# Kernel optimization log

Hardware: AMD Instinct MI355X
Metric: run time of the kernel (lower is better)

## Reference

```python
import jax, jax.numpy as jnp
import numpy as np

B, T, D = 32, 4096, 768
HEADS, DK, DV = 4, 64, 64
REL_W = 32
HIDDEN = 256


def setup_inputs() -> dict:
    key = jax.random.key(0)
    ks = jax.random.split(key, 12)
    H_sent = jax.random.normal(ks[0], (B, T, D), dtype=jnp.float32)
    # realistic padding: each sample has a random valid length in [2048, T]
    lengths = jax.random.randint(ks[1], (B,), 2048, T + 1)
    attention_mask_sent = (jnp.arange(T)[None, :] < lengths[:, None]).astype(jnp.int32)
    noun_pos = jax.random.randint(ks[2], (B,), 0, 2048).astype(jnp.int32)
    pooled_fields = jax.random.normal(ks[3], (B, D), dtype=jnp.float32)
    # xavier-uniform for (heads, d, dk): fan_in=d, fan_out=dk per torch semantics
    def xavier(k, shape, fan_in, fan_out):
        lim = float(np.sqrt(6.0 / (fan_in + fan_out)))
        return jax.random.uniform(k, shape, jnp.float32, -lim, lim)
    WQ = xavier(ks[4], (HEADS, D, DK), D, DK)
    WK = xavier(ks[5], (HEADS, D, DK), D, DK)
    WV = xavier(ks[6], (HEADS, D, DV), D, DV)
    rel_bias = jnp.zeros((HEADS, 2 * REL_W + 1), jnp.float32) + 0.01 * jax.random.normal(ks[7], (HEADS, 2 * REL_W + 1))
    in_proj = D + HEADS * DV + D  # 1792
    proj_w = xavier(ks[8], (HIDDEN, in_proj), in_proj, HIDDEN)
    proj_b = jnp.zeros((HIDDEN,), jnp.float32)
    mlp_w = xavier(ks[9], (2, HIDDEN), HIDDEN, 2)
    mlp_b = jnp.zeros((2,), jnp.float32)
    return {
        "H_sent": H_sent, "attention_mask_sent": attention_mask_sent,
        "noun_pos": noun_pos, "pooled_fields": pooled_fields,
        "WQ": WQ, "WK": WK, "WV": WV, "rel_bias": rel_bias,
        "proj_w": proj_w, "proj_b": proj_b, "mlp_w": mlp_w, "mlp_b": mlp_b,
    }


def reference(H_sent, attention_mask_sent, noun_pos, pooled_fields,
              WQ, WK, WV, rel_bias, proj_w, proj_b, mlp_w, mlp_b):
    b, t, d = H_sent.shape
    heads, _, dk = WQ.shape
    w = (rel_bias.shape[1] - 1) // 2
    # gather single query vector per sample
    h_i = H_sent[jnp.arange(b), noun_pos]  # (B, d)
    Q = jnp.einsum('bd,hdk->bhk', h_i, WQ)        # (B, H, dk)
    K = jnp.einsum('btd,hdk->bthk', H_sent, WK)   # (B, T, H, dk)
    V = jnp.einsum('btd,hdv->bthv', H_sent, WV)   # (B, T, H, dv)
    scores = jnp.einsum('bhk,bthk->bht', Q, K) / jnp.sqrt(jnp.float32(dk))  # (B,H,T)
    # relative-position bias gathered by clamped delta
    delta = jnp.clip(jnp.arange(t)[None, :] - noun_pos[:, None], -w, w) + w  # (B,T)
    rb = rel_bias[:, delta]                        # (H, B, T)
    scores = scores + jnp.transpose(rb, (1, 0, 2))
    scores = jnp.where(attention_mask_sent[:, None, :] == 0, jnp.float32(-1e9), scores)
    alpha = jax.nn.softmax(scores, axis=-1)        # (B, H, T)
    c = jnp.einsum('bht,bthv->bhv', alpha, V).reshape(b, -1)  # (B, H*dv)
    r = jnp.concatenate([h_i, c, pooled_fields], axis=-1)     # (B, d + H*dv + d)
    hdn = jax.nn.gelu(r @ proj_w.T + proj_b, approximate=False)
    logits = hdn @ mlp_w.T + mlp_b                 # (B, 2)
    return logits
```

## Files before the change

### kernel.cpp

```cpp
#include <hip/hip_runtime.h>
#include <math.h>

#define BB 32
#define TT 4096
#define DD 768
#define NH 4
#define RELW 32
#define NREL 65
#define HIDDEN 256
#define INPROJ 1792

#define NCH 32
#define CROWS (TT / NCH)
#define TROWS 8
#define C4 (DD / 4)

#define WAITVM6() asm volatile("s_waitcnt vmcnt(6)" ::: "memory")
#define WAITVM0() asm volatile("s_waitcnt vmcnt(0)" ::: "memory")

__device__ __forceinline__ void gl_lds16(const float* g, float* l) {
    __builtin_amdgcn_global_load_lds(
        (const __attribute__((address_space(1))) float*)(uintptr_t)g,
        (__attribute__((address_space(3))) float*)(uintptr_t)l,
        16, 0, 0);
}

template <int CTRL, int RMASK>
__device__ __forceinline__ float upd0(float x) {
    return __int_as_float(__builtin_amdgcn_update_dpp(
        0, __float_as_int(x), CTRL, RMASK, 0xf, true));
}
__device__ __forceinline__ float wave_sum64(float x) {
    x += upd0<0x111, 0xf>(x);
    x += upd0<0x112, 0xf>(x);
    x += upd0<0x114, 0xf>(x);
    x += upd0<0x118, 0xf>(x);
    x += upd0<0x142, 0xa>(x);
    x += upd0<0x143, 0xc>(x);
    return __int_as_float(__builtin_amdgcn_readlane(__float_as_int(x), 63));
}

__global__ __launch_bounds__(256) void kA(const float* __restrict__ H,
                                          const int* __restrict__ noun_pos,
                                          const float* __restrict__ WQ,
                                          const float* __restrict__ WK,
                                          const float* __restrict__ pooled,
                                          float* __restrict__ R,
                                          float* __restrict__ qk_ws) {
    int b = blockIdx.x / NH, h = blockIdx.x % NH;
    __shared__ float hi_s[DD];
    __shared__ float qpart[4][64];
    __shared__ float q_s[64];
    int tn = noun_pos[b];
    const float* Hrow = H + ((size_t)b * TT + tn) * DD;
    for (int d = threadIdx.x; d < DD; d += 256) {
        float v = Hrow[d];
        hi_s[d] = v;
        if (h == 0) R[(size_t)b * INPROJ + d] = v;
        if (h == 1) R[(size_t)b * INPROJ + DD + NH * 64 + d] = pooled[(size_t)b * DD + d];
    }
    __syncthreads();
    {
        int k = threadIdx.x & 63, ds = threadIdx.x >> 6;
        const float* wq = WQ + (size_t)h * DD * 64 + k;
        float acc = 0.f;
        #pragma unroll 8
        for (int d = ds * 192; d < ds * 192 + 192; ++d) acc += hi_s[d] * wq[(size_t)d * 64];
        qpart[ds][k] = acc;
    }
    __syncthreads();
    if (threadIdx.x < 64)
        q_s[threadIdx.x] = qpart[0][threadIdx.x] + qpart[1][threadIdx.x]
                         + qpart[2][threadIdx.x] + qpart[3][threadIdx.x];
    __syncthreads();
    for (int d = threadIdx.x; d < DD; d += 256) {
        const float* wk = WK + ((size_t)h * DD + d) * 64;
        float acc = 0.f;
        #pragma unroll
        for (int k = 0; k < 64; ++k) acc += q_s[k] * wk[k];
        qk_ws[((size_t)b * NH + h) * DD + d] = acc * 0.125f;
    }
}

#define DOT(ACC, CV, QV) ACC += CV.x*QV.x + CV.y*QV.y + CV.z*QV.z + CV.w*QV.w

#define HUPD(M, L, S0, S1, B0, B1, B2)                                    \
  {                                                                        \
    float nm = fmaxf(M, fmaxf(S0, S1));                                    \
    if (nm > M + 8.0f) {                                                   \
      float sc = __expf(M - nm);                                           \
      L *= sc;                                                             \
      B0.x*=sc; B0.y*=sc; B0.z*=sc; B0.w*=sc;                              \
      B1.x*=sc; B1.y*=sc; B1.z*=sc; B1.w*=sc;                              \
      B2.x*=sc; B2.y*=sc; B2.z*=sc; B2.w*=sc;                              \
      M = nm;                                                              \
    }                                                                      \
    float p0 = __expf(S0 - M), p1 = __expf(S1 - M);                        \
    L += p0 + p1;                                                          \
    B0.x += p0*c0.x + p1*c3.x; B0.y += p0*c0.y + p1*c3.y;                  \
    B0.z += p0*c0.z + p1*c3.z; B0.w += p0*c0.w + p1*c3.w;                  \
    B1.x += p0*c1.x + p1*c4.x; B1.y += p0*c1.y + p1*c4.y;                  \
    B1.z += p0*c1.z + p1*c4.z; B1.w += p0*c1.w + p1*c4.w;                  \
    B2.x += p0*c2.x + p1*c5.x; B2.y += p0*c2.y + p1*c5.y;                  \
    B2.z += p0*c2.z + p1*c5.z; B2.w += p0*c2.w + p1*c5.w;                  \
  }

__global__ __launch_bounds__(256, 3) void kFlash(const float* __restrict__ H,
                                                 const int* __restrict__ mask,
                                                 const int* __restrict__ noun_pos,
                                                 const float* __restrict__ rel_bias,
                                                 const float* __restrict__ qk_ws,
                                                 float* __restrict__ macc,
                                                 float* __restrict__ ml) {
    const int b   = blockIdx.x / NCH;
    const int ch  = blockIdx.x % NCH;
    const int tid = threadIdx.x;
    const int wave = tid >> 6, lane = tid & 63;

    __shared__ float4 Hts[2][TROWS * C4];
    __shared__ float4 rbL[CROWS];
    __shared__ float mls[4][8];
    __shared__ int snl;

    const int t0 = ch * CROWS;
    const int tn = noun_pos[b];

    if (tid == 0) snl = 0;
    __syncthreads();
    if (tid < CROWS) {
        int t = t0 + tid;
        int dl = t - tn; dl = dl < -RELW ? -RELW : (dl > RELW ? RELW : dl);
        int mm = mask[(size_t)b * TT + t];
        float4 rv;
        if (mm) {
            rv.x = rel_bias[0 * NREL + dl + RELW];
            rv.y = rel_bias[1 * NREL + dl + RELW];
            rv.z = rel_bias[2 * NREL + dl + RELW];
            rv.w = rel_bias[3 * NREL + dl + RELW];
            atomicMax(&snl, tid + 1);
        } else {
            rv.x = rv.y = rv.z = rv.w = -2.0e9f;
        }
        rbL[tid] = rv;
    }

    float4 qr[NH][3];
    {
        const float4* qk4 = (const float4*)(qk_ws + (size_t)b * NH * DD);
        #pragma unroll
        for (int h = 0; h < NH; ++h)
            #pragma unroll
            for (int j = 0; j < 3; ++j)
                qr[h][j] = qk4[h * C4 + j * 64 + lane];
    }

    __syncthreads();
    const int NTE = (snl + TROWS - 1) / TROWS;

    if (NTE == 0) {
        float4 z = {0.f, 0.f, 0.f, 0.f};
        float4* mo = (float4*)(macc + (size_t)blockIdx.x * NH * DD);
        int h = tid >> 6, ln = tid & 63;
        #pragma unroll
        for (int j = 0; j < 3; ++j) mo[h * C4 + j * 64 + ln] = z;
        if (tid < NH) {
            float* mp = ml + (size_t)blockIdx.x * NH * 2;
            mp[tid * 2 + 0] = -3.0e38f; mp[tid * 2 + 1] = 0.f;
        }
        return;
    }

    float m0 = -3.0e38f, m1 = -3.0e38f, m2 = -3.0e38f, m3 = -3.0e38f;
    float l0 = 0.f, l1 = 0.f, l2 = 0.f, l3 = 0.f;
    float4 A00{0,0,0,0}, A01{0,0,0,0}, A02{0,0,0,0};
    float4 A10{0,0,0,0}, A11{0,0,0,0}, A12{0,0,0,0};
    float4 A20{0,0,0,0}, A21{0,0,0,0}, A22{0,0,0,0};
    float4 A30{0,0,0,0}, A31{0,0,0,0}, A32{0,0,0,0};

    const float* Hc = H + ((size_t)b * TT + t0) * DD;
    const int woff = wave * 1536;

    {
        float* dst = (float*)&Hts[0][0] + woff;
        const float* src = Hc + woff;
        #pragma unroll
        for (int i = 0; i < 6; ++i)
            gl_lds16(src + i * 256 + lane * 4, dst + i * 256);
    }

    #pragma unroll 1
    for (int t = 0; t < NTE; ++t) {
        const int cur = t & 1;
        if (t + 1 < NTE) {
            float* dst = (float*)&Hts[cur ^ 1][0] + woff;
            const float* src = Hc + (size_t)(t + 1) * TROWS * DD + woff;
            #pragma unroll
            for (int i = 0; i < 6; ++i)
                gl_lds16(src + i * 256 + lane * 4, dst + i * 256);
            WAITVM6();
        } else {
            WAITVM0();
        }
        const float4* Hr = &Hts[cur][0] + wave * 384;
        float4 c0 = Hr[lane],       c1 = Hr[64 + lane],  c2 = Hr[128 + lane];
        float4 c3 = Hr[192 + lane], c4 = Hr[256 + lane], c5 = Hr[320 + lane];

        float s00 = 0, s01 = 0, s02 = 0, s03 = 0;
        float s10 = 0, s11 = 0, s12 = 0, s13 = 0;
        DOT(s00, c0, qr[0][0]); DOT(s00, c1, qr[0][1]); DOT(s00, c2, qr[0][2]);
        DOT(s01, c0, qr[1][0]); DOT(s01, c1, qr[1][1]); DOT(s01, c2, qr[1][2]);
        DOT(s02, c0, qr[2][0]); DOT(s02, c1, qr[2][1]); DOT(s02, c2, qr[2][2]);
        DOT(s03, c0, qr[3][0]); DOT(s03, c1, qr[3][1]); DOT(s03, c2, qr[3][2]);
        DOT(s10, c3, qr[0][0]); DOT(s10, c4, qr[0][1]); DOT(s10, c5, qr[0][2]);
        DOT(s11, c3, qr[1][0]); DOT(s11, c4, qr[1][1]); DOT(s11, c5, qr[1][2]);
        DOT(s12, c3, qr[2][0]); DOT(s12, c4, qr[2][1]); DOT(s12, c5, qr[2][2]);
        DOT(s13, c3, qr[3][0]); DOT(s13, c4, qr[3][1]); DOT(s13, c5, qr[3][2]);
        float r00 = wave_sum64(s00), r01 = wave_sum64(s01);
        float r02 = wave_sum64(s02), r03 = wave_sum64(s03);
        float r10 = wave_sum64(s10), r11 = wave_sum64(s11);
        float r12 = wave_sum64(s12), r13 = wave_sum64(s13);
        float4 rb0 = rbL[t * TROWS + 2 * wave];
        float4 rb1 = rbL[t * TROWS + 2 * wave + 1];
        r00 += rb0.x; r01 += rb0.y; r02 += rb0.z; r03 += rb0.w;
        r10 += rb1.x; r11 += rb1.y; r12 += rb1.z; r13 += rb1.w;
        HUPD(m0, l0, r00, r10, A00, A01, A02);
        HUPD(m1, l1, r01, r11, A10, A11, A12);
        HUPD(m2, l2, r02, r12, A20, A21, A22);
        HUPD(m3, l3, r03, r13, A30, A31, A32);
    }

    __syncthreads();
    float4* scr = &Hts[0][0];
    #pragma unroll
    for (int j = 0; j < 3; ++j) {
        scr[(wave * 4 + 0) * C4 + j * 64 + lane] = j == 0 ? A00 : (j == 1 ? A01 : A02);
        scr[(wave * 4 + 1) * C4 + j * 64 + lane] = j == 0 ? A10 : (j == 1 ? A11 : A12);
        scr[(wave * 4 + 2) * C4 + j * 64 + lane] = j == 0 ? A20 : (j == 1 ? A21 : A22);
        scr[(wave * 4 + 3) * C4 + j * 64 + lane] = j == 0 ? A30 : (j == 1 ? A31 : A32);
    }
    if (lane == 0) {
        mls[wave][0] = m0; mls[wave][1] = l0; mls[wave][2] = m1; mls[wave][3] = l1;
        mls[wave][4] = m2; mls[wave][5] = l2; mls[wave][6] = m3; mls[wave][7] = l3;
    }
    __syncthreads();
    {
        int h = tid >> 6, ln = tid & 63;
        float M = fmaxf(fmaxf(mls[0][h*2], mls[1][h*2]), fmaxf(mls[2][h*2], mls[3][h*2]));
        float w0 = __expf(mls[0][h*2] - M), w1 = __expf(mls[1][h*2] - M);
        float w2 = __expf(mls[2][h*2] - M), w3 = __expf(mls[3][h*2] - M);
        float4* mo = (float4*)(macc + (size_t)blockIdx.x * NH * DD);
        #pragma unroll
        for (int j = 0; j < 3; ++j) {
            float4 v0 = scr[(0*4 + h) * C4 + j * 64 + ln];
            float4 v1 = scr[(1*4 + h) * C4 + j * 64 + ln];
            float4 v2 = scr[(2*4 + h) * C4 + j * 64 + ln];
            float4 v3 = scr[(3*4 + h) * C4 + j * 64 + ln];
            float4 v;
            v.x = w0*v0.x + w1*v1.x + w2*v2.x + w3*v3.x;
            v.y = w0*v0.y + w1*v1.y + w2*v2.y + w3*v3.y;
            v.z = w0*v0.z + w1*v1.z + w2*v2.z + w3*v3.z;
            v.w = w0*v0.w + w1*v1.w + w2*v2.w + w3*v3.w;
            mo[h * C4 + j * 64 + ln] = v;
        }
        if (tid < NH) {
            int hh = tid;
            float Mh = fmaxf(fmaxf(mls[0][hh*2], mls[1][hh*2]), fmaxf(mls[2][hh*2], mls[3][hh*2]));
            float Lh = __expf(mls[0][hh*2] - Mh) * mls[0][hh*2+1]
                     + __expf(mls[1][hh*2] - Mh) * mls[1][hh*2+1]
                     + __expf(mls[2][hh*2] - Mh) * mls[2][hh*2+1]
                     + __expf(mls[3][hh*2] - Mh) * mls[3][hh*2+1];
            float* mp = ml + (size_t)blockIdx.x * NH * 2;
            mp[hh * 2 + 0] = Mh; mp[hh * 2 + 1] = Lh;
        }
    }
}

__global__ __launch_bounds__(256) void kT(const float* __restrict__ pw,
                                          float* __restrict__ pwT) {
    int o = blockIdx.x * 256 + threadIdx.x;
    int j = o / INPROJ, i = o % INPROJ;
    pwT[(size_t)i * HIDDEN + j] = pw[o];
}

__global__ __launch_bounds__(256) void kCombC2(const float* __restrict__ macc,
                                               const float* __restrict__ ml,
                                               const float* __restrict__ WV,
                                               float* __restrict__ R) {
    int b = blockIdx.x / NH, h = blockIdx.x % NH;
    __shared__ float hbar_s[DD];
    __shared__ float mlv[NCH][2];
    __shared__ float cpart[4][64];

    if (threadIdx.x < NCH) {
        const float* mp = ml + ((size_t)(b * NCH + threadIdx.x) * NH + h) * 2;
        mlv[threadIdx.x][0] = mp[0];
        mlv[threadIdx.x][1] = mp[1];
    }
    __syncthreads();
    float M = -3.0e38f;
    #pragma unroll
    for (int c = 0; c < NCH; ++c) M = fmaxf(M, mlv[c][0]);
    float L = 0.f;
    #pragma unroll
    for (int c = 0; c < NCH; ++c) L += __expf(mlv[c][0] - M) * mlv[c][1];
    float invL = 1.f / L;

    #pragma unroll
    for (int j = 0; j < 3; ++j) {
        int d = threadIdx.x + 256 * j;
        float acc = 0.f;
        const float* mc = macc + ((size_t)b * NCH * NH + h) * DD + d;
        #pragma unroll 8
        for (int c = 0; c < NCH; ++c)
            acc += __expf(mlv[c][0] - M) * mc[(size_t)c * NH * DD];
        hbar_s[d] = acc;
    }
    __syncthreads();

    {
        int v = threadIdx.x & 63, ds = threadIdx.x >> 6;
        const float* wv = WV + (size_t)h * DD * 64 + v;
        float acc = 0.f;
        #pragma unroll 8
        for (int d = ds * 192; d < ds * 192 + 192; ++d)
            acc += hbar_s[d] * wv[(size_t)d * 64];
        cpart[ds][v] = acc;
    }
    __syncthreads();
    if (threadIdx.x < 64) {
        float cv = (cpart[0][threadIdx.x] + cpart[1][threadIdx.x]
                  + cpart[2][threadIdx.x] + cpart[3][threadIdx.x]) * invL;
        R[(size_t)b * INPROJ + DD + h * 64 + threadIdx.x] = cv;
    }
}

__global__ __launch_bounds__(256) void kH(const float* __restrict__ R,
                                          const float* __restrict__ pwT,
                                          const float* __restrict__ pb,
                                          const float* __restrict__ mw,
                                          const float* __restrict__ mb,
                                          float* __restrict__ out) {
    int b = blockIdx.x, j = threadIdx.x;
    __shared__ float r_s[INPROJ];
    for (int i = j; i < INPROJ; i += 256) r_s[i] = R[(size_t)b * INPROJ + i];
    __syncthreads();
    float acc = pb[j];
    #pragma unroll 16
    for (int i = 0; i < INPROJ; ++i) acc += r_s[i] * pwT[(size_t)i * HIDDEN + j];
    float hdn = 0.5f * acc * (1.f + erff(acc * 0.70710678118654752f));
    float p0 = hdn * mw[j];
    float p1 = hdn * mw[HIDDEN + j];
    #pragma unroll
    for (int off = 32; off; off >>= 1) {
        p0 += __shfl_xor(p0, off);
        p1 += __shfl_xor(p1, off);
    }
    __shared__ float r0[4], r1[4];
    if ((j & 63) == 0) {
        r0[j >> 6] = p0;
        r1[j >> 6] = p1;
    }
    __syncthreads();
    if (j == 0) {
        out[b * 2 + 0] = r0[0] + r0[1] + r0[2] + r0[3] + mb[0];
        out[b * 2 + 1] = r1[0] + r1[1] + r1[2] + r1[3] + mb[1];
    }
}

extern "C" void kernel_launch(void* const* d_in, const int* in_sizes, int n_in,
                              void* d_out, int out_size, void* d_ws, size_t ws_size,
                              hipStream_t stream) {
    const float* H      = (const float*)d_in[0];
    const int*   mask   = (const int*)d_in[1];
    const int*   noun   = (const int*)d_in[2];
    const float* pooled = (const float*)d_in[3];
    const float* WQ     = (const float*)d_in[4];
    const float* WK     = (const float*)d_in[5];
    const float* WV     = (const float*)d_in[6];
    const float* relb   = (const float*)d_in[7];
    const float* pw     = (const float*)d_in[8];
    const float* pb     = (const float*)d_in[9];
    const float* mw     = (const float*)d_in[10];
    const float* mb     = (const float*)d_in[11];
    float* out = (float*)d_out;

    float* ws    = (float*)d_ws;
    float* R     = ws;
    float* qk    = R + (size_t)BB * INPROJ;
    float* macc  = qk + (size_t)BB * NH * DD;
    float* ml    = macc + (size_t)BB * NCH * NH * DD;
    float* pwT   = ml + (size_t)BB * NCH * NH * 2;

    kA<<<BB * NH, 256, 0, stream>>>(H, noun, WQ, WK, pooled, R, qk);
    kT<<<(HIDDEN * INPROJ) / 256, 256, 0, stream>>>(pw, pwT);
    kFlash<<<BB * NCH, 256, 0, stream>>>(H, mask, noun, relb, qk, macc, ml);
    kCombC2<<<BB * NH, 256, 0, stream>>>(macc, ml, WV, R);
    kH<<<BB, 256, 0, stream>>>(R, pwT, pb, mw, mb, out);
}
```

Before: 154.3 us.

## Drop proj_w transpose kernel and fuse V-projection into tail MLP kernel

Removes the separate transpose kernel for proj_w; the tail kernel now reads proj_w rows directly and reduces each hidden unit with wave-wide dot products. The WV projection moves out of the combine kernel into a new fused tail kernel that also assembles h_i and pooled features. The combine kernel now only writes the normalized hbar. This saves one launch and the transpose traffic, but the tail runs on just 32 blocks with a serial loop over 64 hidden units per wave, which may make it slower.

```diff
diff --git a/kernel.cpp b/kernel.cpp
--- a/kernel.cpp
+++ b/kernel.cpp
@@ -44,8 +44,6 @@
                                           const int* __restrict__ noun_pos,
                                           const float* __restrict__ WQ,
                                           const float* __restrict__ WK,
-                                          const float* __restrict__ pooled,
-                                          float* __restrict__ R,
                                           float* __restrict__ qk_ws) {
     int b = blockIdx.x / NH, h = blockIdx.x % NH;
     __shared__ float hi_s[DD];
@@ -53,12 +51,7 @@
     __shared__ float q_s[64];
     int tn = noun_pos[b];
     const float* Hrow = H + ((size_t)b * TT + tn) * DD;
-    for (int d = threadIdx.x; d < DD; d += 256) {
-        float v = Hrow[d];
-        hi_s[d] = v;
-        if (h == 0) R[(size_t)b * INPROJ + d] = v;
-        if (h == 1) R[(size_t)b * INPROJ + DD + NH * 64 + d] = pooled[(size_t)b * DD + d];
-    }
+    for (int d = threadIdx.x; d < DD; d += 256) hi_s[d] = Hrow[d];
     __syncthreads();
     {
         int k = threadIdx.x & 63, ds = threadIdx.x >> 6;
@@ -230,7 +223,7 @@
     }
 
     __syncthreads();
-    float4* scr = &Hts[0][0];
+    float4* scr = (float4*)&Hts[0][0];
     #pragma unroll
     for (int j = 0; j < 3; ++j) {
         scr[(wave * 4 + 0) * C4 + j * 64 + lane] = j == 0 ? A00 : (j == 1 ? A01 : A02);
@@ -275,22 +268,11 @@
     }
 }
 
-__global__ __launch_bounds__(256) void kT(const float* __restrict__ pw,
-                                          float* __restrict__ pwT) {
-    int o = blockIdx.x * 256 + threadIdx.x;
-    int j = o / INPROJ, i = o % INPROJ;
-    pwT[(size_t)i * HIDDEN + j] = pw[o];
-}
-
-__global__ __launch_bounds__(256) void kCombC2(const float* __restrict__ macc,
-                                               const float* __restrict__ ml,
-                                               const float* __restrict__ WV,
-                                               float* __restrict__ R) {
+__global__ __launch_bounds__(256) void kComb(const float* __restrict__ macc,
+                                             const float* __restrict__ ml,
+                                             float* __restrict__ hbar) {
     int b = blockIdx.x / NH, h = blockIdx.x % NH;
-    __shared__ float hbar_s[DD];
     __shared__ float mlv[NCH][2];
-    __shared__ float cpart[4][64];
-
     if (threadIdx.x < NCH) {
         const float* mp = ml + ((size_t)(b * NCH + threadIdx.x) * NH + h) * 2;
         mlv[threadIdx.x][0] = mp[0];
@@ -304,7 +286,6 @@
     #pragma unroll
     for (int c = 0; c < NCH; ++c) L += __expf(mlv[c][0] - M) * mlv[c][1];
     float invL = 1.f / L;
-
     #pragma unroll
     for (int j = 0; j < 3; ++j) {
         int d = threadIdx.x + 256 * j;
@@ -313,55 +294,74 @@
         #pragma unroll 8
         for (int c = 0; c < NCH; ++c)
             acc += __expf(mlv[c][0] - M) * mc[(size_t)c * NH * DD];
-        hbar_s[d] = acc;
-    }
-    __syncthreads();
-
-    {
-        int v = threadIdx.x & 63, ds = threadIdx.x >> 6;
+        hbar[((size_t)b * NH + h) * DD + d] = acc * invL;
+    }
+}
+
+__global__ __launch_bounds__(256) void kTail(const float* __restrict__ H,
+                                             const int* __restrict__ noun_pos,
+                                             const float* __restrict__ hbar,
+                                             const float* __restrict__ WV,
+                                             const float* __restrict__ pooled,
+                                             const float* __restrict__ pw,
+                                             const float* __restrict__ pb,
+                                             const float* __restrict__ mw,
+                                             const float* __restrict__ mb,
+                                             float* __restrict__ out) {
+    int b = blockIdx.x;
+    int tid = threadIdx.x, wave = tid >> 6, lane = tid & 63;
+    __shared__ float hb_s[NH * DD];
+    __shared__ float r_s[INPROJ];
+    __shared__ float hdn_s[HIDDEN];
+
+    int tn = noun_pos[b];
+    const float* Hrow = H + ((size_t)b * TT + tn) * DD;
+    for (int i = tid; i < NH * DD; i += 256) hb_s[i] = hbar[(size_t)b * NH * DD + i];
+    for (int i = tid; i < DD; i += 256) {
+        r_s[i] = Hrow[i];
+        r_s[DD + NH * 64 + i] = pooled[(size_t)b * DD + i];
+    }
+    __syncthreads();
+    {
+        int h = tid >> 6, v = tid & 63;
         const float* wv = WV + (size_t)h * DD * 64 + v;
+        const float* hb = hb_s + h * DD;
         float acc = 0.f;
         #pragma unroll 8
-        for (int d = ds * 192; d < ds * 192 + 192; ++d)
-            acc += hbar_s[d] * wv[(size_t)d * 64];
-        cpart[ds][v] = acc;
-    }
-    __syncthreads();
-    if (threadIdx.x < 64) {
-        float cv = (cpart[0][threadIdx.x] + cpart[1][threadIdx.x]
-                  + cpart[2][threadIdx.x] + cpart[3][threadIdx.x]) * invL;
-        R[(size_t)b * INPROJ + DD + h * 64 + threadIdx.x] = cv;
-    }
-}
-
-__global__ __launch_bounds__(256) void kH(const float* __restrict__ R,
-                                          const float* __restrict__ pwT,
-                                          const float* __restrict__ pb,
-                                          const float* __restrict__ mw,
-                                          const float* __restrict__ mb,
-                                          float* __restrict__ out) {
-    int b = blockIdx.x, j = threadIdx.x;
-    __shared__ float r_s[INPROJ];
-    for (int i = j; i < INPROJ; i += 256) r_s[i] = R[(size_t)b * INPROJ + i];
-    __syncthreads();
-    float acc = pb[j];
-    #pragma unroll 16
-    for (int i = 0; i < INPROJ; ++i) acc += r_s[i] * pwT[(size_t)i * HIDDEN + j];
-    float hdn = 0.5f * acc * (1.f + erff(acc * 0.70710678118654752f));
-    float p0 = hdn * mw[j];
-    float p1 = hdn * mw[HIDDEN + j];
+        for (int d = 0; d < DD; ++d) acc += hb[d] * wv[(size_t)d * 64];
+        r_s[DD + tid] = acc;
+    }
+    __syncthreads();
+    {
+        for (int jj = 0; jj < 64; ++jj) {
+            int j = jj * 4 + wave;
+            const float* pwr = pw + (size_t)j * INPROJ;
+            float acc = 0.f;
+            #pragma unroll
+            for (int ii = 0; ii < INPROJ / 64; ++ii)
+                acc += r_s[ii * 64 + lane] * pwr[ii * 64 + lane];
+            float s = wave_sum64(acc);
+            if (lane == 0) {
+                s += pb[j];
+                hdn_s[j] = 0.5f * s * (1.f + erff(s * 0.70710678118654752f));
+            }
+        }
+    }
+    __syncthreads();
+    float p0 = hdn_s[tid] * mw[tid];
+    float p1 = hdn_s[tid] * mw[HIDDEN + tid];
     #pragma unroll
     for (int off = 32; off; off >>= 1) {
         p0 += __shfl_xor(p0, off);
         p1 += __shfl_xor(p1, off);
     }
     __shared__ float r0[4], r1[4];
-    if ((j & 63) == 0) {
-        r0[j >> 6] = p0;
-        r1[j >> 6] = p1;
-    }
-    __syncthreads();
-    if (j == 0) {
+    if ((tid & 63) == 0) {
+        r0[tid >> 6] = p0;
+        r1[tid >> 6] = p1;
+    }
+    __syncthreads();
+    if (tid == 0) {
         out[b * 2 + 0] = r0[0] + r0[1] + r0[2] + r0[3] + mb[0];
         out[b * 2 + 1] = r1[0] + r1[1] + r1[2] + r1[3] + mb[1];
     }
@@ -384,16 +384,14 @@
     const float* mb     = (const float*)d_in[11];
     float* out = (float*)d_out;
 
-    float* ws    = (float*)d_ws;
-    float* R     = ws;
-    float* qk    = R + (size_t)BB * INPROJ;
-    float* macc  = qk + (size_t)BB * NH * DD;
-    float* ml    = macc + (size_t)BB * NCH * NH * DD;
-    float* pwT   = ml + (size_t)BB * NCH * NH * 2;
-
-    kA<<<BB * NH, 256, 0, stream>>>(H, noun, WQ, WK, pooled, R, qk);
-    kT<<<(HIDDEN * INPROJ) / 256, 256, 0, stream>>>(pw, pwT);
+    float* ws   = (float*)d_ws;
+    float* qk   = ws;
+    float* macc = qk + (size_t)BB * NH * DD;
+    float* ml   = macc + (size_t)BB * NCH * NH * DD;
+    float* hbar = ml + (size_t)BB * NCH * NH * 2;
+
+    kA<<<BB * NH, 256, 0, stream>>>(H, noun, WQ, WK, qk);
     kFlash<<<BB * NCH, 256, 0, stream>>>(H, mask, noun, relb, qk, macc, ml);
-    kCombC2<<<BB * NH, 256, 0, stream>>>(macc, ml, WV, R);
-    kH<<<BB, 256, 0, stream>>>(R, pwT, pb, mw, mb, out);
-}
+    kComb<<<BB * NH, 256, 0, stream>>>(macc, ml, hbar);
+    kTail<<<BB, 256, 0, stream>>>(H, noun, hbar, WV, pooled, pw, pb, mw, mb, out);
+}
```

Result: slower. 171.4 us (+11.0%).
